# Optimization experiments

Hardware: AMD Instinct MI355X
Metric: run time of the kernel (lower is better)

## Reference

```python
import jax, jax.numpy as jnp
import numpy as np

N_NODES = 100000
N_EDGES = 1600000
IN_F = 64
H1_F = 64
N_CLS = 16
NEG_SLOPE = 0.01  # F.leaky_relu default


def _sage_pool(x, src, dst, n_nodes, W_pool, b_pool, W_self, W_neigh, bias):
    """DGL SAGEConv with aggregator_type='pool'.
    msg = relu(x[src] @ W_pool + b_pool); pooled = max over in-edges per dst
    out = x @ W_self + pooled @ W_neigh + bias (empty segments pooled to 0)."""
    m = jax.nn.relu(x[src] @ W_pool + b_pool)                 # [E, d_in]
    pooled = jax.ops.segment_max(m, dst, num_segments=n_nodes)  # [N, d_in]
    deg = jax.ops.segment_sum(jnp.ones(dst.shape[0], x.dtype), dst,
                              num_segments=n_nodes)           # [N]
    pooled = jnp.where(deg[:, None] > 0, pooled, jnp.zeros((), x.dtype))
    return x @ W_self + pooled @ W_neigh + bias               # [N, d_out]


def setup_inputs() -> dict:
    key = jax.random.key(0)
    ks = jax.random.split(key, 12)
    sc_in = 1.0 / np.sqrt(IN_F)
    sc_h1 = 1.0 / np.sqrt(H1_F)
    inp = {
        "in_feat": jax.random.normal(ks[0], (N_NODES, IN_F), jnp.float32),
        "src": jax.random.randint(ks[1], (N_EDGES,), 0, N_NODES),
        "dst": jax.random.randint(ks[2], (N_EDGES,), 0, N_NODES),
        # layer 1 (in=64 -> out=64)
        "W_pool1": jax.random.normal(ks[3], (IN_F, IN_F), jnp.float32) * sc_in,
        "b_pool1": jnp.zeros((IN_F,), jnp.float32),
        "W_self1": jax.random.normal(ks[4], (IN_F, H1_F), jnp.float32) * sc_in,
        "W_neigh1": jax.random.normal(ks[5], (IN_F, H1_F), jnp.float32) * sc_in,
        "bias1": jnp.zeros((H1_F,), jnp.float32),
        # layer 2 (in=64 -> out=16)
        "W_pool2": jax.random.normal(ks[6], (H1_F, H1_F), jnp.float32) * sc_h1,
        "b_pool2": jnp.zeros((H1_F,), jnp.float32),
        "W_self2": jax.random.normal(ks[7], (H1_F, N_CLS), jnp.float32) * sc_h1,
        "W_neigh2": jax.random.normal(ks[8], (H1_F, N_CLS), jnp.float32) * sc_h1,
        "bias2": jnp.zeros((N_CLS,), jnp.float32),
    }
    return inp


def reference(in_feat, src, dst,
              W_pool1, b_pool1, W_self1, W_neigh1, bias1,
              W_pool2, b_pool2, W_self2, W_neigh2, bias2):
    n = in_feat.shape[0]
    h = _sage_pool(in_feat, src, dst, n, W_pool1, b_pool1, W_self1, W_neigh1, bias1)
    h = jnp.where(h >= 0, h, NEG_SLOPE * h)  # leaky_relu
    out = _sage_pool(h, src, dst, n, W_pool2, b_pool2, W_self2, W_neigh2, bias2)
    return out
```

## Files before the change

### kernel.cpp

```cpp
#include <hip/hip_runtime.h>
#include <cstddef>
#include <cstdint>

#define CAP 64
#define SCAP 40
#define CHUNK2 4096
#define PR 5632

typedef _Float16 h2 __attribute__((ext_vector_type(2)));
static __device__ __forceinline__ h2 h2max(h2 a, h2 b) {
  return __builtin_elementwise_max(a, b);
}
static __device__ __forceinline__ h2 bch2(int u) { return __builtin_bit_cast(h2, u); }
static __device__ __forceinline__ int packrelu(float a, float b) {
  h2 t; t.x = (_Float16)fmaxf(a, 0.f); t.y = (_Float16)fmaxf(b, 0.f);
  return __builtin_bit_cast(int, t);
}
static __device__ __forceinline__ int packleaky(float a, float b) {
  float la = (a >= 0.f) ? a : 0.01f * a;
  float lb = (b >= 0.f) ? b : 0.01f * b;
  h2 t; t.x = (_Float16)la; t.y = (_Float16)lb;
  return __builtin_bit_cast(int, t);
}
static __device__ __forceinline__ float fdot2f(h2 a, h2 b, float c) {
#if __has_builtin(__builtin_amdgcn_fdot2)
  return __builtin_amdgcn_fdot2(a, b, c, false);
#else
  return c + (float)a.x * (float)b.x + (float)a.y * (float)b.y;
#endif
}

__global__ __launch_bounds__(256) void k_build(const int* __restrict__ src,
                                               const int* __restrict__ dst,
                                               unsigned int* __restrict__ pairs,
                                               int* __restrict__ cnt2,
                                               int E, int P, int NC,
                                               const float* __restrict__ X,
                                               const float* __restrict__ W,
                                               const float* __restrict__ bias,
                                               _Float16* __restrict__ Z, int n) {
  __shared__ __attribute__((aligned(16))) char smem[24576];
  int tid = threadIdx.x;
  if ((int)blockIdx.x < NC) {
    int* hcnt = (int*)smem;
    for (int p = tid; p < 512; p += 256) hcnt[p] = 0;
    __syncthreads();
    int chunk = blockIdx.x;
    int e0 = chunk * CHUNK2;
    unsigned int* pbase = pairs + (size_t)chunk * P * SCAP;
    #pragma unroll
    for (int k = 0; k < CHUNK2 / 256; k++) {
      int e = e0 + k * 256 + tid;
      if (e < E) {
        int d = dst[e], s = src[e];
        int p = d >> 8;
        int slot = atomicAdd(&hcnt[p], 1);
        if (slot < SCAP)
          pbase[p * SCAP + slot] = (unsigned)s | ((unsigned)(d & 255) << 17);
      }
    }
    __syncthreads();
    int* cbase = cnt2 + (size_t)chunk * P;
    for (int p = tid; p < P; p += 256) {
      int c = hcnt[p];
      cbase[p] = (c < SCAP) ? c : SCAP;
    }
    return;
  }
  h2* sW  = (h2*)smem;
  h2* sXT = (h2*)(smem + 8192);
  #pragma unroll
  for (int it = 0; it < 8; it++) {
    int idx = it * 256 + tid;
    int kp = idx >> 6, c = idx & 63;
    h2 t;
    t.x = (_Float16)W[(2 * kp) * 64 + c];
    t.y = (_Float16)W[(2 * kp + 1) * 64 + c];
    sW[kp * 64 + c] = t;
  }
  int node0 = (blockIdx.x - NC) * 128;
  #pragma unroll
  for (int it = 0; it < 8; it++) {
    int idx = it * 256 + tid;
    int row = idx & 127, c4 = idx >> 7;
    int node = node0 + row;
    float4 v = make_float4(0.f, 0.f, 0.f, 0.f);
    if (node < n) v = ((const float4*)(X + (size_t)node * 64))[c4];
    h2 a; a.x = (_Float16)v.x; a.y = (_Float16)v.y;
    h2 d; d.x = (_Float16)v.z; d.y = (_Float16)v.w;
    sXT[(2 * c4 + 0) * 128 + row] = a;
    sXT[(2 * c4 + 1) * 128 + row] = d;
  }
  __syncthreads();
  int lane = tid & 63;
  int cg = tid >> 6;
  float acc0[16], acc1[16];
  #pragma unroll
  for (int c4 = 0; c4 < 4; c4++) {
    float4 bv = ((const float4*)bias)[cg * 4 + c4];
    acc0[c4 * 4 + 0] = bv.x; acc0[c4 * 4 + 1] = bv.y;
    acc0[c4 * 4 + 2] = bv.z; acc0[c4 * 4 + 3] = bv.w;
    acc1[c4 * 4 + 0] = bv.x; acc1[c4 * 4 + 1] = bv.y;
    acc1[c4 * 4 + 2] = bv.z; acc1[c4 * 4 + 3] = bv.w;
  }
  #pragma unroll 8
  for (int kp = 0; kp < 32; kp++) {
    h2 x0 = sXT[kp * 128 + lane];
    h2 x1 = sXT[kp * 128 + lane + 64];
    const int4* wq = (const int4*)(sW + kp * 64 + cg * 16);
    #pragma unroll
    for (int q4 = 0; q4 < 4; q4++) {
      int4 wv = wq[q4];
      h2 w0 = bch2(wv.x), w1 = bch2(wv.y), w2 = bch2(wv.z), w3 = bch2(wv.w);
      acc0[q4 * 4 + 0] = fdot2f(x0, w0, acc0[q4 * 4 + 0]);
      acc0[q4 * 4 + 1] = fdot2f(x0, w1, acc0[q4 * 4 + 1]);
      acc0[q4 * 4 + 2] = fdot2f(x0, w2, acc0[q4 * 4 + 2]);
      acc0[q4 * 4 + 3] = fdot2f(x0, w3, acc0[q4 * 4 + 3]);
      acc1[q4 * 4 + 0] = fdot2f(x1, w0, acc1[q4 * 4 + 0]);
      acc1[q4 * 4 + 1] = fdot2f(x1, w1, acc1[q4 * 4 + 1]);
      acc1[q4 * 4 + 2] = fdot2f(x1, w2, acc1[q4 * 4 + 2]);
      acc1[q4 * 4 + 3] = fdot2f(x1, w3, acc1[q4 * 4 + 3]);
    }
  }
  int nodeA = node0 + lane;
  int nodeB = node0 + lane + 64;
  if (nodeA < n) {
    int4 o0, o1;
    o0.x = packrelu(acc0[0], acc0[1]);   o0.y = packrelu(acc0[2], acc0[3]);
    o0.z = packrelu(acc0[4], acc0[5]);   o0.w = packrelu(acc0[6], acc0[7]);
    o1.x = packrelu(acc0[8], acc0[9]);   o1.y = packrelu(acc0[10], acc0[11]);
    o1.z = packrelu(acc0[12], acc0[13]); o1.w = packrelu(acc0[14], acc0[15]);
    char* rp = (char*)Z + (size_t)nodeA * 128 + cg * 32;
    ((int4*)rp)[0] = o0; ((int4*)rp)[1] = o1;
  }
  if (nodeB < n) {
    int4 o0, o1;
    o0.x = packrelu(acc1[0], acc1[1]);   o0.y = packrelu(acc1[2], acc1[3]);
    o0.z = packrelu(acc1[4], acc1[5]);   o0.w = packrelu(acc1[6], acc1[7]);
    o1.x = packrelu(acc1[8], acc1[9]);   o1.y = packrelu(acc1[10], acc1[11]);
    o1.z = packrelu(acc1[12], acc1[13]); o1.w = packrelu(acc1[14], acc1[15]);
    char* rp = (char*)Z + (size_t)nodeB * 128 + cg * 32;
    ((int4*)rp)[0] = o0; ((int4*)rp)[1] = o1;
  }
}

__global__ __launch_bounds__(256) void k_fill3(const unsigned int* __restrict__ pairs,
                                               const int* __restrict__ cnt2,
                                               int* __restrict__ rowcnt,
                                               int* __restrict__ bucket,
                                               int n, int NC, int P) {
  __shared__ int sbucket[256 * CAP];
  __shared__ int scnt[256];
  __shared__ int soff[256];
  __shared__ int scnt2[512];
  int tid = threadIdx.x;
  int p = blockIdx.x;
  scnt[tid] = 0;
  for (int c = tid; c < NC; c += 256) scnt2[c] = cnt2[(size_t)c * P + p];
  __syncthreads();
  int total = NC * SCAP;
  for (int t = tid; t < total; t += 256) {
    int chunk = t / SCAP;
    int slot = t - chunk * SCAP;
    if (slot < scnt2[chunk]) {
      unsigned int u = pairs[(size_t)chunk * P * SCAP + p * SCAP + slot];
      int s = (int)(u & 0x1FFFFu);
      int dlow = (int)(u >> 17);
      int sl = atomicAdd(&scnt[dlow], 1);
      if (sl < CAP)
        sbucket[dlow * CAP + sl] = s;
    }
  }
  __syncthreads();
  int c = scnt[tid];
  if (c > CAP) c = CAP;
  int ca = (c + 3) & ~3;
  soff[tid] = ca;
  __syncthreads();
  #pragma unroll
  for (int off = 1; off < 256; off <<= 1) {
    int t = (tid >= off) ? soff[tid - off] : 0;
    __syncthreads();
    soff[tid] += t;
    __syncthreads();
  }
  int local = soff[tid] - ca;
  int node = (p << 8) + tid;
  int gbase = p * PR + local;
  if (node < n)
    rowcnt[node] = gbase | (c << 22);
  for (int j = 0; j < c; j += 4) {
    int4 v = *(const int4*)&sbucket[tid * CAP + j];
    *(int4*)&bucket[gbase + j] = v;
  }
}

static __device__ __forceinline__ h2 gather_one(const char* zb,
                                                const int* __restrict__ bucket,
                                                int rc) {
  int c = rc >> 22;
  const int* bk = bucket + (rc & 0x3FFFFF);
  h2 acc = (h2)(_Float16)0;
  int j = 0;
  for (; j + 8 <= c; j += 8) {
    int4 a = *(const int4*)(bk + j);
    int4 d = *(const int4*)(bk + j + 4);
    int u0 = *(const int*)(zb + (size_t)a.x * 128);
    int u1 = *(const int*)(zb + (size_t)a.y * 128);
    int u2 = *(const int*)(zb + (size_t)a.z * 128);
    int u3 = *(const int*)(zb + (size_t)a.w * 128);
    int u4 = *(const int*)(zb + (size_t)d.x * 128);
    int u5 = *(const int*)(zb + (size_t)d.y * 128);
    int u6 = *(const int*)(zb + (size_t)d.z * 128);
    int u7 = *(const int*)(zb + (size_t)d.w * 128);
    h2 m0 = h2max(bch2(u0), bch2(u1));
    h2 m1 = h2max(bch2(u2), bch2(u3));
    h2 m2 = h2max(bch2(u4), bch2(u5));
    h2 m3 = h2max(bch2(u6), bch2(u7));
    acc = h2max(acc, h2max(h2max(m0, m1), h2max(m2, m3)));
  }
  if (j + 4 <= c) {
    int4 a = *(const int4*)(bk + j);
    int u0 = *(const int*)(zb + (size_t)a.x * 128);
    int u1 = *(const int*)(zb + (size_t)a.y * 128);
    int u2 = *(const int*)(zb + (size_t)a.z * 128);
    int u3 = *(const int*)(zb + (size_t)a.w * 128);
    acc = h2max(acc, h2max(h2max(bch2(u0), bch2(u1)), h2max(bch2(u2), bch2(u3))));
    j += 4;
  }
  if (j + 2 <= c) {
    int2 a = *(const int2*)(bk + j);
    int u0 = *(const int*)(zb + (size_t)a.x * 128);
    int u1 = *(const int*)(zb + (size_t)a.y * 128);
    acc = h2max(acc, h2max(bch2(u0), bch2(u1)));
    j += 2;
  }
  if (j < c) {
    int u0 = *(const int*)(zb + (size_t)bk[j] * 128);
    acc = h2max(acc, bch2(u0));
  }
  return acc;
}

__global__ __launch_bounds__(256) void k_gather2(const _Float16* __restrict__ Z,
                                                 const int* __restrict__ bucket,
                                                 const int* __restrict__ rowcnt,
                                                 _Float16* __restrict__ pooled, int n) {
  int t = blockIdx.x * 256 + threadIdx.x;
  int pairid = t >> 5;
  int sub = t & 31;
  int nA = pairid * 2;
  int nB = nA + 1;
  if (nA >= n) return;
  const char* zb = (const char*)Z + sub * 4;
  int rcA = rowcnt[nA];
  h2 accA, accB;
  if (nB < n) {
    int rcB = rowcnt[nB];
    accA = gather_one(zb, bucket, rcA);
    accB = gather_one(zb, bucket, rcB);
    *(int*)((char*)pooled + (size_t)nA * 128 + sub * 4) = __builtin_bit_cast(int, accA);
    *(int*)((char*)pooled + (size_t)nB * 128 + sub * 4) = __builtin_bit_cast(int, accB);
  } else {
    accA = gather_one(zb, bucket, rcA);
    *(int*)((char*)pooled + (size_t)nA * 128 + sub * 4) = __builtin_bit_cast(int, accA);
  }
}

__global__ __launch_bounds__(256) void k_hl(const float* __restrict__ X,
                                            const _Float16* __restrict__ P,
                                            const float* __restrict__ Ws,
                                            const float* __restrict__ Wn,
                                            const float* __restrict__ bias,
                                            const float* __restrict__ Wp2,
                                            const float* __restrict__ bp2,
                                            _Float16* __restrict__ H,
                                            _Float16* __restrict__ Z2, int n) {
  __shared__ __attribute__((aligned(16))) h2 sWs[32 * 64];
  __shared__ __attribute__((aligned(16))) h2 sWn[32 * 64];
  __shared__ __attribute__((aligned(16))) h2 sXT[32 * 128];
  __shared__ __attribute__((aligned(16))) h2 sPT[32 * 128];
  int tid = threadIdx.x;
  #pragma unroll
  for (int it = 0; it < 8; it++) {
    int idx = it * 256 + tid;
    int kp = idx >> 6, c = idx & 63;
    h2 t1, t2;
    t1.x = (_Float16)Ws[(2 * kp) * 64 + c];
    t1.y = (_Float16)Ws[(2 * kp + 1) * 64 + c];
    t2.x = (_Float16)Wn[(2 * kp) * 64 + c];
    t2.y = (_Float16)Wn[(2 * kp + 1) * 64 + c];
    sWs[kp * 64 + c] = t1;
    sWn[kp * 64 + c] = t2;
  }
  int node0 = blockIdx.x * 128;
  #pragma unroll
  for (int it = 0; it < 8; it++) {
    int idx = it * 256 + tid;
    int row = idx & 127, c4 = idx >> 7;
    int node = node0 + row;
    float4 v = make_float4(0.f, 0.f, 0.f, 0.f);
    if (node < n) v = ((const float4*)(X + (size_t)node * 64))[c4];
    h2 a; a.x = (_Float16)v.x; a.y = (_Float16)v.y;
    h2 d; d.x = (_Float16)v.z; d.y = (_Float16)v.w;
    sXT[(2 * c4 + 0) * 128 + row] = a;
    sXT[(2 * c4 + 1) * 128 + row] = d;
  }
  #pragma unroll
  for (int it = 0; it < 4; it++) {
    int idx = it * 256 + tid;
    int row = idx & 127, q = idx >> 7;
    int node = node0 + row;
    int4 u = make_int4(0, 0, 0, 0);
    if (node < n) u = ((const int4*)((const char*)P + (size_t)node * 128))[q];
    sPT[(4 * q + 0) * 128 + row] = bch2(u.x);
    sPT[(4 * q + 1) * 128 + row] = bch2(u.y);
    sPT[(4 * q + 2) * 128 + row] = bch2(u.z);
    sPT[(4 * q + 3) * 128 + row] = bch2(u.w);
  }
  __syncthreads();
  int lane = tid & 63;
  int cg = tid >> 6;
  float acc0[16], acc1[16];
  #pragma unroll
  for (int c4 = 0; c4 < 4; c4++) {
    float4 bv = ((const float4*)bias)[cg * 4 + c4];
    acc0[c4 * 4 + 0] = bv.x; acc0[c4 * 4 + 1] = bv.y;
    acc0[c4 * 4 + 2] = bv.z; acc0[c4 * 4 + 3] = bv.w;
    acc1[c4 * 4 + 0] = bv.x; acc1[c4 * 4 + 1] = bv.y;
    acc1[c4 * 4 + 2] = bv.z; acc1[c4 * 4 + 3] = bv.w;
  }
  #pragma unroll 8
  for (int kp = 0; kp < 32; kp++) {
    h2 x0 = sXT[kp * 128 + lane];
    h2 x1 = sXT[kp * 128 + lane + 64];
    h2 p0 = sPT[kp * 128 + lane];
    h2 p1 = sPT[kp * 128 + lane + 64];
    const int4* wsq = (const int4*)(sWs + kp * 64 + cg * 16);
    const int4* wnq = (const int4*)(sWn + kp * 64 + cg * 16);
    #pragma unroll
    for (int q4 = 0; q4 < 4; q4++) {
      int4 a = wsq[q4];
      int4 d = wnq[q4];
      h2 s0 = bch2(a.x), s1 = bch2(a.y), s2 = bch2(a.z), s3 = bch2(a.w);
      h2 n0 = bch2(d.x), n1 = bch2(d.y), n2 = bch2(d.z), n3 = bch2(d.w);
      acc0[q4 * 4 + 0] = fdot2f(x0, s0, acc0[q4 * 4 + 0]);
      acc0[q4 * 4 + 1] = fdot2f(x0, s1, acc0[q4 * 4 + 1]);
      acc0[q4 * 4 + 2] = fdot2f(x0, s2, acc0[q4 * 4 + 2]);
      acc0[q4 * 4 + 3] = fdot2f(x0, s3, acc0[q4 * 4 + 3]);
      acc0[q4 * 4 + 0] = fdot2f(p0, n0, acc0[q4 * 4 + 0]);
      acc0[q4 * 4 + 1] = fdot2f(p0, n1, acc0[q4 * 4 + 1]);
      acc0[q4 * 4 + 2] = fdot2f(p0, n2, acc0[q4 * 4 + 2]);
      acc0[q4 * 4 + 3] = fdot2f(p0, n3, acc0[q4 * 4 + 3]);
      acc1[q4 * 4 + 0] = fdot2f(x1, s0, acc1[q4 * 4 + 0]);
      acc1[q4 * 4 + 1] = fdot2f(x1, s1, acc1[q4 * 4 + 1]);
      acc1[q4 * 4 + 2] = fdot2f(x1, s2, acc1[q4 * 4 + 2]);
      acc1[q4 * 4 + 3] = fdot2f(x1, s3, acc1[q4 * 4 + 3]);
      acc1[q4 * 4 + 0] = fdot2f(p1, n0, acc1[q4 * 4 + 0]);
      acc1[q4 * 4 + 1] = fdot2f(p1, n1, acc1[q4 * 4 + 1]);
      acc1[q4 * 4 + 2] = fdot2f(p1, n2, acc1[q4 * 4 + 2]);
      acc1[q4 * 4 + 3] = fdot2f(p1, n3, acc1[q4 * 4 + 3]);
    }
  }
  int ha[8], hb[8];
  #pragma unroll
  for (int j = 0; j < 8; j++) {
    ha[j] = packleaky(acc0[2 * j], acc0[2 * j + 1]);
    hb[j] = packleaky(acc1[2 * j], acc1[2 * j + 1]);
  }
  int nodeA = node0 + lane;
  int nodeB = node0 + lane + 64;
  __syncthreads();
  #pragma unroll
  for (int j = 0; j < 8; j++) {
    sXT[(cg * 8 + j) * 128 + lane]      = bch2(ha[j]);
    sXT[(cg * 8 + j) * 128 + lane + 64] = bch2(hb[j]);
  }
  #pragma unroll
  for (int it = 0; it < 8; it++) {
    int idx = it * 256 + tid;
    int kp = idx >> 6, c = idx & 63;
    h2 t;
    t.x = (_Float16)Wp2[(2 * kp) * 64 + c];
    t.y = (_Float16)Wp2[(2 * kp + 1) * 64 + c];
    sWs[kp * 64 + c] = t;
  }
  if (nodeA < n) {
    char* rp = (char*)H + (size_t)nodeA * 128 + cg * 32;
    ((int4*)rp)[0] = make_int4(ha[0], ha[1], ha[2], ha[3]);
    ((int4*)rp)[1] = make_int4(ha[4], ha[5], ha[6], ha[7]);
  }
  if (nodeB < n) {
    char* rp = (char*)H + (size_t)nodeB * 128 + cg * 32;
    ((int4*)rp)[0] = make_int4(hb[0], hb[1], hb[2], hb[3]);
    ((int4*)rp)[1] = make_int4(hb[4], hb[5], hb[6], hb[7]);
  }
  __syncthreads();
  float c0[16], c1[16];
  #pragma unroll
  for (int c4 = 0; c4 < 4; c4++) {
    float4 bv = ((const float4*)bp2)[cg * 4 + c4];
    c0[c4 * 4 + 0] = bv.x; c0[c4 * 4 + 1] = bv.y;
    c0[c4 * 4 + 2] = bv.z; c0[c4 * 4 + 3] = bv.w;
    c1[c4 * 4 + 0] = bv.x; c1[c4 * 4 + 1] = bv.y;
    c1[c4 * 4 + 2] = bv.z; c1[c4 * 4 + 3] = bv.w;
  }
  #pragma unroll 8
  for (int kp = 0; kp < 32; kp++) {
    h2 x0 = sXT[kp * 128 + lane];
    h2 x1 = sXT[kp * 128 + lane + 64];
    const int4* wq = (const int4*)(sWs + kp * 64 + cg * 16);
    #pragma unroll
    for (int q4 = 0; q4 < 4; q4++) {
      int4 wv = wq[q4];
      h2 w0 = bch2(wv.x), w1 = bch2(wv.y), w2 = bch2(wv.z), w3 = bch2(wv.w);
      c0[q4 * 4 + 0] = fdot2f(x0, w0, c0[q4 * 4 + 0]);
      c0[q4 * 4 + 1] = fdot2f(x0, w1, c0[q4 * 4 + 1]);
      c0[q4 * 4 + 2] = fdot2f(x0, w2, c0[q4 * 4 + 2]);
      c0[q4 * 4 + 3] = fdot2f(x0, w3, c0[q4 * 4 + 3]);
      c1[q4 * 4 + 0] = fdot2f(x1, w0, c1[q4 * 4 + 0]);
      c1[q4 * 4 + 1] = fdot2f(x1, w1, c1[q4 * 4 + 1]);
      c1[q4 * 4 + 2] = fdot2f(x1, w2, c1[q4 * 4 + 2]);
      c1[q4 * 4 + 3] = fdot2f(x1, w3, c1[q4 * 4 + 3]);
    }
  }
  if (nodeA < n) {
    int4 o0, o1;
    o0.x = packrelu(c0[0], c0[1]);   o0.y = packrelu(c0[2], c0[3]);
    o0.z = packrelu(c0[4], c0[5]);   o0.w = packrelu(c0[6], c0[7]);
    o1.x = packrelu(c0[8], c0[9]);   o1.y = packrelu(c0[10], c0[11]);
    o1.z = packrelu(c0[12], c0[13]); o1.w = packrelu(c0[14], c0[15]);
    char* rp = (char*)Z2 + (size_t)nodeA * 128 + cg * 32;
    ((int4*)rp)[0] = o0; ((int4*)rp)[1] = o1;
  }
  if (nodeB < n) {
    int4 o0, o1;
    o0.x = packrelu(c1[0], c1[1]);   o0.y = packrelu(c1[2], c1[3]);
    o0.z = packrelu(c1[4], c1[5]);   o0.w = packrelu(c1[6], c1[7]);
    o1.x = packrelu(c1[8], c1[9]);   o1.y = packrelu(c1[10], c1[11]);
    o1.z = packrelu(c1[12], c1[13]); o1.w = packrelu(c1[14], c1[15]);
    char* rp = (char*)Z2 + (size_t)nodeB * 128 + cg * 32;
    ((int4*)rp)[0] = o0; ((int4*)rp)[1] = o1;
  }
}

__global__ __launch_bounds__(256) void k_gather_out(const _Float16* __restrict__ Z,
                                                    const int* __restrict__ bucket,
                                                    const int* __restrict__ rowcnt,
                                                    const _Float16* __restrict__ Hrow,
                                                    const float* __restrict__ Ws,
                                                    const float* __restrict__ Wn,
                                                    const float* __restrict__ bias,
                                                    float* __restrict__ OUT, int n) {
  __shared__ __attribute__((aligned(16))) h2 sWs[32 * 16];
  __shared__ __attribute__((aligned(16))) h2 sWn[32 * 16];
  __shared__ __attribute__((aligned(16))) h2 sH[8][32];
  __shared__ __attribute__((aligned(16))) h2 sP[8][32];
  __shared__ float sB[16];
  int tid = threadIdx.x;
  #pragma unroll
  for (int it = 0; it < 2; it++) {
    int idx = it * 256 + tid;
    int kp = idx >> 4, c = idx & 15;
    h2 t1, t2;
    t1.x = (_Float16)Ws[(2 * kp) * 16 + c];
    t1.y = (_Float16)Ws[(2 * kp + 1) * 16 + c];
    t2.x = (_Float16)Wn[(2 * kp) * 16 + c];
    t2.y = (_Float16)Wn[(2 * kp + 1) * 16 + c];
    sWs[kp * 16 + c] = t1;
    sWn[kp * 16 + c] = t2;
  }
  if (tid < 16) sB[tid] = bias[tid];
  int nodeBase = blockIdx.x * 8;
  if (tid < 64) {
    int nd = nodeBase + (tid >> 3);
    int q = tid & 7;
    int4 u = make_int4(0, 0, 0, 0);
    if (nd < n) u = ((const int4*)((const char*)Hrow + (size_t)nd * 128))[q];
    ((int4*)&sH[tid >> 3][0])[q] = u;
  }
  int en = tid >> 5;
  int node = nodeBase + en;
  int sub = tid & 31;
  h2 acc = (h2)(_Float16)0;
  if (node < n)
    acc = gather_one((const char*)Z + sub * 4, bucket, rowcnt[node]);
  sP[en][sub] = acc;
  __syncthreads();
  int col = tid & 15;
  int kh = (tid >> 4) & 1;
  float v = 0.f;
  #pragma unroll
  for (int j = 0; j < 16; j++) {
    int kp = kh * 16 + j;
    v = fdot2f(sH[en][kp], sWs[kp * 16 + col], v);
    v = fdot2f(sP[en][kp], sWn[kp * 16 + col], v);
  }
  v += __shfl_xor(v, 16);
  if (kh == 0 && node < n)
    OUT[(size_t)node * 16 + col] = v + sB[col];
}

extern "C" void kernel_launch(void* const* d_in, const int* in_sizes, int n_in,
                              void* d_out, int out_size, void* d_ws, size_t ws_size,
                              hipStream_t stream) {
  const float* X   = (const float*)d_in[0];
  const int*   src = (const int*)d_in[1];
  const int*   dst = (const int*)d_in[2];
  const float* Wp1 = (const float*)d_in[3];
  const float* bp1 = (const float*)d_in[4];
  const float* Ws1 = (const float*)d_in[5];
  const float* Wn1 = (const float*)d_in[6];
  const float* b1  = (const float*)d_in[7];
  const float* Wp2 = (const float*)d_in[8];
  const float* bp2 = (const float*)d_in[9];
  const float* Ws2 = (const float*)d_in[10];
  const float* Wn2 = (const float*)d_in[11];
  const float* b2  = (const float*)d_in[12];
  float* OUT = (float*)d_out;

  const int n = in_sizes[0] / 64;
  const int E = in_sizes[1];
  const int P = (n + 255) >> 8;
  const int NC = (E + CHUNK2 - 1) / CHUNK2;

  char* w = (char*)d_ws;
  auto alloc = [&](size_t bytes) -> char* {
    char* p = w;
    w += (bytes + 255) & ~(size_t)255;
    return p;
  };
  int*  rowcnt = (int*)alloc((size_t)n * 4);
  int*  bucket = (int*)alloc((size_t)P * PR * 4);
  int*  cnt2   = (int*)alloc((size_t)NC * P * 4);
  size_t pairs_b = (size_t)NC * P * SCAP * 4;
  size_t h_b     = (size_t)n * 64 * 2;
  char* ali = alloc(pairs_b > h_b ? pairs_b : h_b);
  unsigned int* pairs = (unsigned int*)ali;
  _Float16*     h16   = (_Float16*)ali;
  _Float16* zh     = (_Float16*)alloc((size_t)n * 64 * 2);
  _Float16* pooled = (_Float16*)alloc((size_t)n * 64 * 2);
  (void)ws_size; (void)n_in; (void)out_size;

  const int nbT  = (n + 127) / 128;
  const int nbG2 = (n * 16 + 255) / 256;
  const int nbG8 = (n + 7) / 8;

  k_build<<<NC + nbT, 256, 0, stream>>>(src, dst, pairs, cnt2, E, P, NC,
                                        X, Wp1, bp1, zh, n);
  k_fill3<<<P, 256, 0, stream>>>(pairs, cnt2, rowcnt, bucket, n, NC, P);
  k_gather2<<<nbG2, 256, 0, stream>>>(zh, bucket, rowcnt, pooled, n);
  k_hl<<<nbT, 256, 0, stream>>>(X, pooled, Ws1, Wn1, b1, Wp2, bp2, h16, zh, n);
  k_gather_out<<<nbG8, 256, 0, stream>>>(zh, bucket, rowcnt, h16,
                                         Ws2, Wn2, b2, OUT, n);
}
```

Baseline: 180.4 us.

## Compact per-chunk edge pairs using histogram prefix-sum offsets instead of fixed slots

The edge bucketing kernel now makes two passes per chunk. The first builds a per-partition histogram and an exclusive scan, so each chunk writes its pairs densely into a CHUNK2-sized region rather than fixed 40-slot partition bins. Offset and count are packed into cnt2, and the fill kernel reads from the compacted offsets with a 48-entry per-chunk bound. This shrinks the pairs buffer and makes its writes denser. In exchange, build re-reads dst and adds a block scan with extra barriers, and the fill loop runs more idle iterations.

Result: slower. 185.2 us (+2.7%).

```diff
diff --git a/kernel.cpp b/kernel.cpp
--- a/kernel.cpp
+++ b/kernel.cpp
@@ -3,7 +3,7 @@
 #include <cstdint>
 
 #define CAP 64
-#define SCAP 40
+#define SCAPI 48
 #define CHUNK2 4096
 #define PR 5632
 
@@ -43,11 +43,39 @@
   int tid = threadIdx.x;
   if ((int)blockIdx.x < NC) {
     int* hcnt = (int*)smem;
+    int* soff = (int*)(smem + 2048);
+    int* sv   = (int*)(smem + 4096);
     for (int p = tid; p < 512; p += 256) hcnt[p] = 0;
     __syncthreads();
     int chunk = blockIdx.x;
     int e0 = chunk * CHUNK2;
-    unsigned int* pbase = pairs + (size_t)chunk * P * SCAP;
+    #pragma unroll
+    for (int k = 0; k < CHUNK2 / 256; k++) {
+      int e = e0 + k * 256 + tid;
+      if (e < E) atomicAdd(&hcnt[dst[e] >> 8], 1);
+    }
+    __syncthreads();
+    int c0 = hcnt[2 * tid], c1 = hcnt[2 * tid + 1];
+    int pairsum = c0 + c1;
+    sv[tid] = pairsum;
+    __syncthreads();
+    #pragma unroll
+    for (int off = 1; off < 256; off <<= 1) {
+      int tv = (tid >= off) ? sv[tid - off] : 0;
+      __syncthreads();
+      sv[tid] += tv;
+      __syncthreads();
+    }
+    int excl = sv[tid] - pairsum;
+    soff[2 * tid] = excl;
+    soff[2 * tid + 1] = excl + c0;
+    __syncthreads();
+    int* cbase = cnt2 + (size_t)chunk * P;
+    for (int p = tid; p < P; p += 256)
+      cbase[p] = soff[p] | (hcnt[p] << 16);
+    for (int p = tid; p < 512; p += 256) hcnt[p] = 0;
+    __syncthreads();
+    unsigned int* pbase = pairs + (size_t)chunk * CHUNK2;
     #pragma unroll
     for (int k = 0; k < CHUNK2 / 256; k++) {
       int e = e0 + k * 256 + tid;
@@ -55,15 +83,8 @@
         int d = dst[e], s = src[e];
         int p = d >> 8;
         int slot = atomicAdd(&hcnt[p], 1);
-        if (slot < SCAP)
-          pbase[p * SCAP + slot] = (unsigned)s | ((unsigned)(d & 255) << 17);
+        pbase[soff[p] + slot] = (unsigned)s | ((unsigned)(d & 255) << 17);
       }
-    }
-    __syncthreads();
-    int* cbase = cnt2 + (size_t)chunk * P;
-    for (int p = tid; p < P; p += 256) {
-      int c = hcnt[p];
-      cbase[p] = (c < SCAP) ? c : SCAP;
     }
     return;
   }
@@ -158,12 +179,14 @@
   scnt[tid] = 0;
   for (int c = tid; c < NC; c += 256) scnt2[c] = cnt2[(size_t)c * P + p];
   __syncthreads();
-  int total = NC * SCAP;
+  int total = NC * SCAPI;
   for (int t = tid; t < total; t += 256) {
-    int chunk = t / SCAP;
-    int slot = t - chunk * SCAP;
-    if (slot < scnt2[chunk]) {
-      unsigned int u = pairs[(size_t)chunk * P * SCAP + p * SCAP + slot];
+    int chunk = t / SCAPI;
+    int slot = t - chunk * SCAPI;
+    int pk = scnt2[chunk];
+    int m = pk >> 16;
+    if (slot < m) {
+      unsigned int u = pairs[(size_t)chunk * CHUNK2 + (pk & 0xFFFF) + slot];
       int s = (int)(u & 0x1FFFFu);
       int dlow = (int)(u >> 17);
       int sl = atomicAdd(&scnt[dlow], 1);
@@ -533,7 +556,7 @@
   int*  rowcnt = (int*)alloc((size_t)n * 4);
   int*  bucket = (int*)alloc((size_t)P * PR * 4);
   int*  cnt2   = (int*)alloc((size_t)NC * P * 4);
-  size_t pairs_b = (size_t)NC * P * SCAP * 4;
+  size_t pairs_b = (size_t)NC * CHUNK2 * 4;
   size_t h_b     = (size_t)n * 64 * 2;
   char* ali = alloc(pairs_b > h_b ? pairs_b : h_b);
   unsigned int* pairs = (unsigned int*)ali;
```

## Split fill kernel into two half-partition blocks and vectorize weight staging

Applied to the files above, without the earlier changes.

The bucket-fill kernel now launches two blocks per 256-node partition. Each block handles one half of the destination nodes, so shared memory per block drops and roughly twice as many blocks can run. Every block still scans all pairs of its partition and discards half, which doubles global reads of the pairs array, and the half-size region assumes no half needs more than 2816 bucket slots. Weight staging to LDS in the build and hidden-layer kernels now uses float4 loads and int4 stores instead of scalar loads.

Result: no change. 181.9 us (+0.8%).

```diff
diff --git a/kernel.cpp b/kernel.cpp
--- a/kernel.cpp
+++ b/kernel.cpp
@@ -6,6 +6,7 @@
 #define SCAP 40
 #define CHUNK2 4096
 #define PR 5632
+#define HPR 2816
 
 typedef _Float16 h2 __attribute__((ext_vector_type(2)));
 static __device__ __forceinline__ h2 h2max(h2 a, h2 b) {
@@ -28,6 +29,26 @@
 #else
   return c + (float)a.x * (float)b.x + (float)a.y * (float)b.y;
 #endif
+}
+
+static __device__ __forceinline__ void stageW64(h2* dstLds,
+                                                const float* __restrict__ W,
+                                                int tid) {
+  #pragma unroll
+  for (int it = 0; it < 2; it++) {
+    int idx = it * 256 + tid;
+    int kp = idx >> 4;
+    int c4 = idx & 15;
+    float4 a = ((const float4*)(W + (2 * kp) * 64))[c4];
+    float4 b = ((const float4*)(W + (2 * kp + 1) * 64))[c4];
+    h2 h0; h0.x = (_Float16)a.x; h0.y = (_Float16)b.x;
+    h2 h1; h1.x = (_Float16)a.y; h1.y = (_Float16)b.y;
+    h2 hv; hv.x = (_Float16)a.z; hv.y = (_Float16)b.z;
+    h2 h3; h3.x = (_Float16)a.w; h3.y = (_Float16)b.w;
+    int4 o = make_int4(__builtin_bit_cast(int, h0), __builtin_bit_cast(int, h1),
+                       __builtin_bit_cast(int, hv), __builtin_bit_cast(int, h3));
+    *(int4*)(dstLds + kp * 64 + c4 * 4) = o;
+  }
 }
 
 __global__ __launch_bounds__(256) void k_build(const int* __restrict__ src,
@@ -69,15 +90,7 @@
   }
   h2* sW  = (h2*)smem;
   h2* sXT = (h2*)(smem + 8192);
-  #pragma unroll
-  for (int it = 0; it < 8; it++) {
-    int idx = it * 256 + tid;
-    int kp = idx >> 6, c = idx & 63;
-    h2 t;
-    t.x = (_Float16)W[(2 * kp) * 64 + c];
-    t.y = (_Float16)W[(2 * kp + 1) * 64 + c];
-    sW[kp * 64 + c] = t;
-  }
+  stageW64(sW, W, tid);
   int node0 = (blockIdx.x - NC) * 128;
   #pragma unroll
   for (int it = 0; it < 8; it++) {
@@ -149,13 +162,14 @@
                                                int* __restrict__ rowcnt,
                                                int* __restrict__ bucket,
                                                int n, int NC, int P) {
-  __shared__ int sbucket[256 * CAP];
-  __shared__ int scnt[256];
+  __shared__ int sbucket[128 * CAP];
+  __shared__ int scnt[128];
   __shared__ int soff[256];
   __shared__ int scnt2[512];
   int tid = threadIdx.x;
-  int p = blockIdx.x;
-  scnt[tid] = 0;
+  int p = blockIdx.x >> 1;
+  int half = blockIdx.x & 1;
+  if (tid < 128) scnt[tid] = 0;
   for (int c = tid; c < NC; c += 256) scnt2[c] = cnt2[(size_t)c * P + p];
   __syncthreads();
   int total = NC * SCAP;
@@ -164,18 +178,24 @@
     int slot = t - chunk * SCAP;
     if (slot < scnt2[chunk]) {
       unsigned int u = pairs[(size_t)chunk * P * SCAP + p * SCAP + slot];
-      int s = (int)(u & 0x1FFFFu);
       int dlow = (int)(u >> 17);
-      int sl = atomicAdd(&scnt[dlow], 1);
-      if (sl < CAP)
-        sbucket[dlow * CAP + sl] = s;
-    }
-  }
-  __syncthreads();
-  int c = scnt[tid];
-  if (c > CAP) c = CAP;
+      if ((dlow >> 7) == half) {
+        int s = (int)(u & 0x1FFFFu);
+        int li = dlow & 127;
+        int sl = atomicAdd(&scnt[li], 1);
+        if (sl < CAP)
+          sbucket[li * CAP + sl] = s;
+      }
+    }
+  }
+  __syncthreads();
+  int c = 0;
+  if (tid < 128) {
+    c = scnt[tid];
+    if (c > CAP) c = CAP;
+  }
   int ca = (c + 3) & ~3;
-  soff[tid] = ca;
+  soff[tid] = (tid < 128) ? ca : 0;
   __syncthreads();
   #pragma unroll
   for (int off = 1; off < 256; off <<= 1) {
@@ -184,14 +204,16 @@
     soff[tid] += t;
     __syncthreads();
   }
-  int local = soff[tid] - ca;
-  int node = (p << 8) + tid;
-  int gbase = p * PR + local;
-  if (node < n)
-    rowcnt[node] = gbase | (c << 22);
-  for (int j = 0; j < c; j += 4) {
-    int4 v = *(const int4*)&sbucket[tid * CAP + j];
-    *(int4*)&bucket[gbase + j] = v;
+  if (tid < 128) {
+    int local = soff[tid] - ca;
+    int node = (p << 8) + (half << 7) + tid;
+    int gbase = p * PR + half * HPR + local;
+    if (node < n)
+      rowcnt[node] = gbase | (c << 22);
+    for (int j = 0; j < c; j += 4) {
+      int4 v = *(const int4*)&sbucket[tid * CAP + j];
+      *(int4*)&bucket[gbase + j] = v;
+    }
   }
 }
 
@@ -281,18 +303,8 @@
   __shared__ __attribute__((aligned(16))) h2 sXT[32 * 128];
   __shared__ __attribute__((aligned(16))) h2 sPT[32 * 128];
   int tid = threadIdx.x;
-  #pragma unroll
-  for (int it = 0; it < 8; it++) {
-    int idx = it * 256 + tid;
-    int kp = idx >> 6, c = idx & 63;
-    h2 t1, t2;
-    t1.x = (_Float16)Ws[(2 * kp) * 64 + c];
-    t1.y = (_Float16)Ws[(2 * kp + 1) * 64 + c];
-    t2.x = (_Float16)Wn[(2 * kp) * 64 + c];
-    t2.y = (_Float16)Wn[(2 * kp + 1) * 64 + c];
-    sWs[kp * 64 + c] = t1;
-    sWn[kp * 64 + c] = t2;
-  }
+  stageW64(sWs, Ws, tid);
+  stageW64(sWn, Wn, tid);
   int node0 = blockIdx.x * 128;
   #pragma unroll
   for (int it = 0; it < 8; it++) {
@@ -376,15 +388,7 @@
     sXT[(cg * 8 + j) * 128 + lane]      = bch2(ha[j]);
     sXT[(cg * 8 + j) * 128 + lane + 64] = bch2(hb[j]);
   }
-  #pragma unroll
-  for (int it = 0; it < 8; it++) {
-    int idx = it * 256 + tid;
-    int kp = idx >> 6, c = idx & 63;
-    h2 t;
-    t.x = (_Float16)Wp2[(2 * kp) * 64 + c];
-    t.y = (_Float16)Wp2[(2 * kp + 1) * 64 + c];
-    sWs[kp * 64 + c] = t;
-  }
+  stageW64(sWs, Wp2, tid);
   if (nodeA < n) {
     char* rp = (char*)H + (size_t)nodeA * 128 + cg * 32;
     ((int4*)rp)[0] = make_int4(ha[0], ha[1], ha[2], ha[3]);
@@ -548,7 +552,7 @@
 
   k_build<<<NC + nbT, 256, 0, stream>>>(src, dst, pairs, cnt2, E, P, NC,
                                         X, Wp1, bp1, zh, n);
-  k_fill3<<<P, 256, 0, stream>>>(pairs, cnt2, rowcnt, bucket, n, NC, P);
+  k_fill3<<<2 * P, 256, 0, stream>>>(pairs, cnt2, rowcnt, bucket, n, NC, P);
   k_gather2<<<nbG2, 256, 0, stream>>>(zh, bucket, rowcnt, pooled, n);
   k_hl<<<nbT, 256, 0, stream>>>(X, pooled, Ws1, Wn1, b1, Wp2, bp2, h16, zh, n);
   k_gather_out<<<nbG8, 256, 0, stream>>>(zh, bucket, rowcnt, h16,
```
